# Kernel optimization log

Measured on AMD Instinct MI355X. Metric: run time of the kernel, lower is better.

Reference implementation:

```python
import jax, jax.numpy as jnp
import numpy as np

N_NODES = 100000
N_EDGES = 200000
D_LAT = 64
D_ENC = 32
N_FEAT = 2  # output features 'p', 'q'
D_IN = 2 * D_LAT + D_LAT + D_ENC + D_ENC  # 256
D_HID = 64


def setup_inputs() -> dict:
    key = jax.random.key(0)
    ks = jax.random.split(key, 12)
    return {
        "edge_array": jax.random.normal(ks[0], (N_EDGES, 4), dtype=jnp.float32),
        "h_local": jax.random.normal(ks[1], (N_NODES, D_LAT), dtype=jnp.float32),
        "h_global": jax.random.normal(ks[2], (1, D_LAT), dtype=jnp.float32),
        "enc_local": jax.random.normal(ks[3], (N_EDGES, D_ENC), dtype=jnp.float32),
        "enc_global": jax.random.normal(ks[4], (1, D_ENC), dtype=jnp.float32),
        "W1": jax.random.normal(ks[5], (N_FEAT, D_IN, D_HID), dtype=jnp.float32) / np.sqrt(D_IN),
        "b1": jnp.zeros((N_FEAT, D_HID), dtype=jnp.float32),
        "W2": jax.random.normal(ks[6], (N_FEAT, D_HID, D_HID), dtype=jnp.float32) / np.sqrt(D_HID),
        "b2": jnp.zeros((N_FEAT, D_HID), dtype=jnp.float32),
        "W3": jax.random.normal(ks[7], (N_FEAT, D_HID, 1), dtype=jnp.float32) / np.sqrt(D_HID),
        "b3": jnp.zeros((N_FEAT, 1), dtype=jnp.float32),
        "addr_from": jax.random.randint(ks[8], (N_EDGES,), 0, N_NODES, dtype=jnp.int32),
        "addr_to": jax.random.randint(ks[9], (N_EDGES,), 0, N_NODES, dtype=jnp.int32),
    }


def reference(edge_array, h_local, h_global, enc_local, enc_global,
              W1, b1, W2, b2, W3, b3, addr_from, addr_to):
    n = enc_local.shape[0]
    # gather node latents per address (drop/fill-0 semantics for out-of-range)
    g_from = h_local.at[addr_from].get(mode='fill', fill_value=0.0)  # [n, D_LAT]
    g_to = h_local.at[addr_to].get(mode='fill', fill_value=0.0)      # [n, D_LAT]
    # concat: [latents..., h_global*ones, enc_local, enc_global*ones]
    x = jnp.concatenate([
        g_from, g_to,
        jnp.broadcast_to(h_global, (n, h_global.shape[1])),
        enc_local,
        jnp.broadcast_to(enc_global, (n, enc_global.shape[1])),
    ], axis=1)  # [n, D_IN]
    # stacked per-feature MLPs (one MLP per output feature)
    h1 = jax.nn.leaky_relu(jnp.einsum('ni,fio->fno', x, W1) + b1[:, None, :])
    h2 = jax.nn.leaky_relu(jnp.einsum('fni,fio->fno', h1, W2) + b2[:, None, :])
    out = (jnp.einsum('fni,fio->fno', h2, W3) + b3[:, None, :])[..., 0]  # [F, n]
    isnan_mask = jnp.isnan(edge_array[:, 0])
    return jnp.where(isnan_mask[None, :], jnp.nan, out)
```

## Files before the change

kernel.cpp:

```cpp
#include <hip/hip_runtime.h>


#define OFF_W1 0
#define OFF_W2 40960
#define OFF_B1 57344
#define OFF_B2 57856
#define OFF_W3 58368
#define OFF_B3 58880
#define OFF_EA0 59392
#define NWAVE 8
#define LDS_TOTAL 58944
#define PREP_W_BLOCKS 114

typedef __attribute__((ext_vector_type(8))) short bf16x8;
typedef __attribute__((ext_vector_type(4))) float f32x4;

__device__ inline short f2bf(float f) {
    unsigned u = __builtin_bit_cast(unsigned, f);
    u += 0x7FFFu + ((u >> 16) & 1u);
    return (short)(u >> 16);
}

__device__ inline float4 ld4(const float* p, bool v) {
    if (v) return *(const float4*)p;
    return make_float4(0.f, 0.f, 0.f, 0.f);
}

__device__ inline unsigned cvt_pk(float lo, float hi) {
    unsigned r;
    asm("v_cvt_pk_bf16_f32 %0, %1, %2" : "=v"(r) : "v"(lo), "v"(hi));
    return r;
}

__device__ inline bf16x8 pack8(float4 a, float4 b) {
    union { bf16x8 v; unsigned u[4]; } r;
    r.u[0] = cvt_pk(a.x, a.y);
    r.u[1] = cvt_pk(a.z, a.w);
    r.u[2] = cvt_pk(b.x, b.y);
    r.u[3] = cvt_pk(b.z, b.w);
    return r.v;
}

__global__ void prep_all(const float* __restrict__ W1, const float* __restrict__ b1,
                         const float* __restrict__ W2, const float* __restrict__ b2,
                         const float* __restrict__ W3, const float* __restrict__ b3,
                         const float* __restrict__ h_global, const float* __restrict__ enc_global,
                         const float* __restrict__ edge_array, const float* __restrict__ h_local,
                         int n_edges, int n8,
                         float* __restrict__ ea0, short* __restrict__ hbf,
                         char* __restrict__ ws) {
    int b = blockIdx.x;
    if (b >= PREP_W_BLOCKS) {
        int rb = b - PREP_W_BLOCKS;
        int eb = (n_edges + 255) >> 8;
        if (rb < eb) {
            int e = rb * 256 + threadIdx.x;
            if (e < n_edges) ea0[e] = ((const float4*)edge_array)[e].x;
        } else {
            int i = (rb - eb) * 256 + threadIdx.x;
            if (i < n8) {
                float4 a = ((const float4*)h_local)[2 * i];
                float4 c = ((const float4*)h_local)[2 * i + 1];
                ((bf16x8*)hbf)[i] = pack8(a, c);
            } else if (i < n8 + 8) {
                ((bf16x8*)hbf)[i] = (bf16x8){0, 0, 0, 0, 0, 0, 0, 0};
            }
        }
        return;
    }
    int idx = b * 256 + threadIdx.x;
    short* w1f = (short*)(ws + OFF_W1);
    short* w2f = (short*)(ws + OFF_W2);
    float* bp1 = (float*)(ws + OFF_B1);
    float* bp2 = (float*)(ws + OFF_B2);
    float* wp3 = (float*)(ws + OFF_W3);
    float* bp3 = (float*)(ws + OFF_B3);
    if (idx < 20480) {
        int f = idx / 10240, r0 = idx % 10240;
        int kk = r0 / 2048, r1 = r0 % 2048;
        int mm = r1 / 512,  r2 = r1 % 512;
        int l = r2 / 8,     j = r2 % 8;
        int kt = kk * 32 + (l >> 4) * 8 + j;
        int r = (kt < 128) ? kt : kt + 64;
        int c = mm * 16 + (l & 15);
        w1f[idx] = f2bf(W1[(f * 256 + r) * 64 + c]);
    } else if (idx < 28672) {
        int i2 = idx - 20480;
        int f = i2 / 4096, r0 = i2 % 4096;
        int kk = r0 / 2048, r1 = r0 % 2048;
        int mm = r1 / 512,  r2 = r1 % 512;
        int l = r2 / 8,     j = r2 % 8;
        int k = kk * 32 + (l >> 4) * 8 + j;
        int c = mm * 16 + (l & 15);
        w2f[i2] = f2bf(W2[(f * 64 + k) * 64 + c]);
    } else if (idx < 28800) {
        int i3 = idx - 28672; int f = i3 / 64, o = i3 % 64;
        float s = b1[f * 64 + o];
        for (int t = 0; t < 64; ++t) s += h_global[t] * W1[(f * 256 + 128 + t) * 64 + o];
        for (int t = 0; t < 32; ++t) s += enc_global[t] * W1[(f * 256 + 224 + t) * 64 + o];
        bp1[i3] = s;
    } else if (idx < 28928) {
        int i4 = idx - 28800; bp2[i4] = b2[i4];
    } else if (idx < 29056) {
        int i5 = idx - 28928; wp3[i5] = W3[i5];
    } else if (idx < 29058) {
        bp3[idx - 29056] = b3[idx - 29056];
    }
}

struct Tile { bf16x8 a0, a1, a2, a3; float4 e0, e1; float ea; };

template<bool HBF>
__device__ inline void gather_tile(int tbase, int n_edges, int n_nodes,
        const int* __restrict__ addr_from, const int* __restrict__ addr_to,
        const float* __restrict__ h_local, const short* __restrict__ hbf,
        const float* __restrict__ enc_local, const float* __restrict__ edge_array,
        const float* __restrict__ ea0, int col16, int g, Tile& T) {
    int e = tbase + col16;
    if (HBF) {
        int ec = e < n_edges ? e : n_edges - 1;
        int af = addr_from[ec], at = addr_to[ec];
        unsigned ra = (unsigned)af < (unsigned)n_nodes ? (unsigned)af : (unsigned)n_nodes;
        unsigned rt = (unsigned)at < (unsigned)n_nodes ? (unsigned)at : (unsigned)n_nodes;
        const short* pf = hbf + (size_t)ra * 64 + g * 8;
        const short* pt = hbf + (size_t)rt * 64 + g * 8;
        T.a0 = *(const bf16x8*)pf; T.a1 = *(const bf16x8*)(pf + 32);
        T.a2 = *(const bf16x8*)pt; T.a3 = *(const bf16x8*)(pt + 32);
        const float* pe = enc_local + (size_t)ec * 32 + g * 8;
        T.e0 = *(const float4*)pe; T.e1 = *(const float4*)(pe + 4);
        T.ea = ea0[ec];
    } else {
        bool ev = e < n_edges;
        int af = ev ? addr_from[e] : -1;
        int at = ev ? addr_to[e] : -1;
        bool afv = (unsigned)af < (unsigned)n_nodes;
        bool atv = (unsigned)at < (unsigned)n_nodes;
        const float* pf = h_local + (size_t)(afv ? af : 0) * 64 + g * 8;
        const float* pt = h_local + (size_t)(atv ? at : 0) * 64 + g * 8;
        T.a0 = pack8(ld4(pf, afv),      ld4(pf + 4, afv));
        T.a1 = pack8(ld4(pf + 32, afv), ld4(pf + 36, afv));
        T.a2 = pack8(ld4(pt, atv),      ld4(pt + 4, atv));
        T.a3 = pack8(ld4(pt + 32, atv), ld4(pt + 36, atv));
        const float* pe = enc_local + (size_t)(ev ? e : 0) * 32 + g * 8;
        T.e0 = ld4(pe, ev); T.e1 = ld4(pe + 4, ev);
        T.ea = ev ? edge_array[4 * e] : 0.f;
    }
}

template<bool HBF>
__global__ __launch_bounds__(512, 4) void main_kernel(
        const float* __restrict__ edge_array, const float* __restrict__ h_local,
        const float* __restrict__ enc_local,
        const int* __restrict__ addr_from, const int* __restrict__ addr_to,
        const char* __restrict__ ws, const float* __restrict__ ea0,
        const short* __restrict__ hbf, float* __restrict__ out,
        int n_edges, int n_nodes) {
    __shared__ __align__(16) char lds[LDS_TOTAL];
    const int tid = threadIdx.x;
    const int lane = tid & 63, wave = tid >> 6;
    const int col16 = lane & 15, g = lane >> 4;
    const int g4 = g * 4;
    const bool hi = g >= 2;
    const int srcA = col16 + 32 * (g & 1);
    const int srcB = srcA + 16;
    const int ntiles = (n_edges + 15) >> 4;
    const int wstride = gridDim.x * NWAVE;

    int t = blockIdx.x * NWAVE + wave;
    bool valid = t < ntiles;
    Tile cur;
    if (valid)
        gather_tile<HBF>(t * 16, n_edges, n_nodes, addr_from, addr_to, h_local,
                         hbf, enc_local, edge_array, ea0, col16, g, cur);

    #pragma unroll
    for (int it = 0; it < 7; ++it)
        ((float4*)lds)[it * 512 + tid] = ((const float4*)ws)[it * 512 + tid];
    if (tid < 100)
        ((float4*)(lds + 57344))[tid] = ((const float4*)(ws + 57344))[tid];
    __syncthreads();

    const float b3v0 = ((const float*)(lds + OFF_B3))[0];
    const float b3v1 = ((const float*)(lds + OFF_B3))[1];

    while (valid) {
        bf16x8 a1[5] = {cur.a0, cur.a1, cur.a2, cur.a3, pack8(cur.e0, cur.e1)};
        float ea = cur.ea;
        int tb = t * 16;

        int tn = t + wstride;
        bool vnext = tn < ntiles;
        if (vnext)
            gather_tile<HBF>(tn * 16, n_edges, n_nodes, addr_from, addr_to, h_local,
                             hbf, enc_local, edge_array, ea0, col16, g, cur);

        #pragma unroll
        for (int f = 0; f < 2; ++f) {
            f32x4 acc1[4];
            #pragma unroll
            for (int mm = 0; mm < 4; ++mm)
                acc1[mm] = *(const f32x4*)(lds + OFF_B1 + (f * 64 + mm * 16 + g4) * 4);
            #pragma unroll
            for (int kk = 0; kk < 5; ++kk)
                #pragma unroll
                for (int mm = 0; mm < 4; ++mm) {
                    bf16x8 w = *(const bf16x8*)(lds + OFF_W1 + ((f * 5 + kk) * 4 + mm) * 1024 + lane * 16);
                    acc1[mm] = __builtin_amdgcn_mfma_f32_16x16x32_bf16(w, a1[kk], acc1[mm], 0, 0, 0);
                }

            unsigned pk[4][2];
            #pragma unroll
            for (int mm = 0; mm < 4; ++mm) {
                float v0 = acc1[mm][0], v1 = acc1[mm][1];
                float v2 = acc1[mm][2], v3 = acc1[mm][3];
                v0 = fmaxf(v0, 0.01f * v0); v1 = fmaxf(v1, 0.01f * v1);
                v2 = fmaxf(v2, 0.01f * v2); v3 = fmaxf(v3, 0.01f * v3);
                pk[mm][0] = cvt_pk(v0, v1);
                pk[mm][1] = cvt_pk(v2, v3);
            }

            f32x4 acc2[4];
            #pragma unroll
            for (int mm = 0; mm < 4; ++mm)
                acc2[mm] = *(const f32x4*)(lds + OFF_B2 + (f * 64 + mm * 16 + g4) * 4);
            #pragma unroll
            for (int kk2 = 0; kk2 < 2; ++kk2) {
                unsigned mL0 = pk[2 * kk2][0],     mL1 = pk[2 * kk2][1];
                unsigned mH0 = pk[2 * kk2 + 1][0], mH1 = pk[2 * kk2 + 1][1];
                unsigned t0L = (unsigned)__shfl((int)mL0, srcA, 64);
                unsigned t0H = (unsigned)__shfl((int)mH0, srcA, 64);
                unsigned t1L = (unsigned)__shfl((int)mL1, srcA, 64);
                unsigned t1H = (unsigned)__shfl((int)mH1, srcA, 64);
                unsigned t2L = (unsigned)__shfl((int)mL0, srcB, 64);
                unsigned t2H = (unsigned)__shfl((int)mH0, srcB, 64);
                unsigned t3L = (unsigned)__shfl((int)mL1, srcB, 64);
                unsigned t3H = (unsigned)__shfl((int)mH1, srcB, 64);
                union { bf16x8 v; unsigned u[4]; } bb;
                bb.u[0] = hi ? t0H : t0L;
                bb.u[1] = hi ? t1H : t1L;
                bb.u[2] = hi ? t2H : t2L;
                bb.u[3] = hi ? t3H : t3L;
                #pragma unroll
                for (int mm = 0; mm < 4; ++mm) {
                    bf16x8 w = *(const bf16x8*)(lds + OFF_W2 + ((f * 2 + kk2) * 4 + mm) * 1024 + lane * 16);
                    acc2[mm] = __builtin_amdgcn_mfma_f32_16x16x32_bf16(w, bb.v, acc2[mm], 0, 0, 0);
                }
            }

            float p = 0.f;
            #pragma unroll
            for (int mm = 0; mm < 4; ++mm) {
                f32x4 wv = *(const f32x4*)(lds + OFF_W3 + (f * 64 + mm * 16 + g4) * 4);
                #pragma unroll
                for (int jj = 0; jj < 4; ++jj) {
                    float h = acc2[mm][jj];
                    h = fmaxf(h, 0.01f * h);
                    p = fmaf(h, wv[jj], p);
                }
            }
            p += __shfl_xor(p, 16, 64);
            p += __shfl_xor(p, 32, 64);
            if (lane < 16) {
                int ee = tb + lane;
                if (ee < n_edges) {
                    float val = p + (f == 0 ? b3v0 : b3v1);
                    if (__builtin_isnan(ea)) val = __builtin_nanf("");
                    out[f * n_edges + ee] = val;
                }
            }
        }

        t = tn; valid = vnext;
    }
}

extern "C" void kernel_launch(void* const* d_in, const int* in_sizes, int n_in,
                              void* d_out, int out_size, void* d_ws, size_t ws_size,
                              hipStream_t stream) {
    const float* edge_array = (const float*)d_in[0];
    const float* h_local    = (const float*)d_in[1];
    const float* h_global   = (const float*)d_in[2];
    const float* enc_local  = (const float*)d_in[3];
    const float* enc_global = (const float*)d_in[4];
    const float* W1 = (const float*)d_in[5];
    const float* b1 = (const float*)d_in[6];
    const float* W2 = (const float*)d_in[7];
    const float* b2 = (const float*)d_in[8];
    const float* W3 = (const float*)d_in[9];
    const float* b3 = (const float*)d_in[10];
    const int* addr_from = (const int*)d_in[11];
    const int* addr_to   = (const int*)d_in[12];
    int n_edges = in_sizes[11];
    int n_nodes = in_sizes[1] / 64;
    int n8 = n_nodes * 8;
    char* ws = (char*)d_ws;

    size_t off_ea0 = OFF_EA0;
    size_t off_hbf = (off_ea0 + (size_t)n_edges * 4 + 255) & ~(size_t)255;
    size_t need = off_hbf + (size_t)(n_nodes + 1) * 128;
    bool use_hbf = ws_size >= need;
    float* ea0 = (float*)(ws + off_ea0);
    short* hbf = (short*)(ws + off_hbf);

    int eb = (n_edges + 255) / 256;
    int hb = (n8 + 8 + 255) / 256;
    int prep_blocks = PREP_W_BLOCKS + (use_hbf ? eb + hb : 0);
    hipLaunchKernelGGL(prep_all, dim3(prep_blocks), dim3(256), 0, stream,
                       W1, b1, W2, b2, W3, b3, h_global, enc_global,
                       edge_array, h_local, n_edges, n8, ea0, hbf, ws);

    int ntiles = (n_edges + 15) / 16;
    int nblk = 512;
    if (nblk * NWAVE > ntiles) nblk = (ntiles + NWAVE - 1) / NWAVE;
    if (use_hbf) {
        hipLaunchKernelGGL((main_kernel<true>), dim3(nblk), dim3(512), 0, stream,
                           edge_array, h_local, enc_local, addr_from, addr_to,
                           ws, ea0, hbf, (float*)d_out, n_edges, n_nodes);
    } else {
        hipLaunchKernelGGL((main_kernel<false>), dim3(nblk), dim3(512), 0, stream,
                           edge_array, h_local, enc_local, addr_from, addr_to,
                           ws, ea0, hbf, (float*)d_out, n_edges, n_nodes);
    }
}
```

Measured before the change: 37.24 us.

## Switch MLP to 32x32x16 MFMA tiles with 32-edge wave tiles

Moves the per-wave MLP from 16x16x32 to 32x32x16 bf16 MFMA, so each wave processes 32 edges per iteration. The W1 and W2 pre-swizzle layouts change to match, and the layer-2 operand exchange is reduced to xor-32 shuffles. The prefetch now covers only the address indices for the next tile, and the node rows are loaded in the current iteration, which may expose more gather latency. Accumulator register use grows, and ea0 is now always prepared, even on the fallback path.

```diff
diff --git a/kernel.cpp b/kernel.cpp
--- a/kernel.cpp
+++ b/kernel.cpp
@@ -14,6 +14,7 @@
 
 typedef __attribute__((ext_vector_type(8))) short bf16x8;
 typedef __attribute__((ext_vector_type(4))) float f32x4;
+typedef __attribute__((ext_vector_type(16))) float f32x16;
 
 __device__ inline short f2bf(float f) {
     unsigned u = __builtin_bit_cast(unsigned, f);
@@ -40,6 +41,8 @@
     r.u[3] = cvt_pk(b.z, b.w);
     return r.v;
 }
+
+__device__ inline float lrelu(float x) { return fmaxf(x, 0.01f * x); }
 
 __global__ void prep_all(const float* __restrict__ W1, const float* __restrict__ b1,
                          const float* __restrict__ W2, const float* __restrict__ b2,
@@ -77,21 +80,21 @@
     float* bp3 = (float*)(ws + OFF_B3);
     if (idx < 20480) {
         int f = idx / 10240, r0 = idx % 10240;
-        int kk = r0 / 2048, r1 = r0 % 2048;
+        int kk = r0 / 1024, r1 = r0 % 1024;
         int mm = r1 / 512,  r2 = r1 % 512;
         int l = r2 / 8,     j = r2 % 8;
-        int kt = kk * 32 + (l >> 4) * 8 + j;
+        int kt = kk * 16 + (l >> 5) * 8 + j;
         int r = (kt < 128) ? kt : kt + 64;
-        int c = mm * 16 + (l & 15);
+        int c = mm * 32 + (l & 31);
         w1f[idx] = f2bf(W1[(f * 256 + r) * 64 + c]);
     } else if (idx < 28672) {
         int i2 = idx - 20480;
         int f = i2 / 4096, r0 = i2 % 4096;
-        int kk = r0 / 2048, r1 = r0 % 2048;
+        int kk2 = r0 / 1024, r1 = r0 % 1024;
         int mm = r1 / 512,  r2 = r1 % 512;
         int l = r2 / 8,     j = r2 % 8;
-        int k = kk * 32 + (l >> 4) * 8 + j;
-        int c = mm * 16 + (l & 15);
+        int k = kk2 * 16 + (l >> 5) * 8 + j;
+        int c = mm * 32 + (l & 31);
         w2f[i2] = f2bf(W2[(f * 64 + k) * 64 + c]);
     } else if (idx < 28800) {
         int i3 = idx - 28672; int f = i3 / 64, o = i3 % 64;
@@ -108,49 +111,9 @@
     }
 }
 
-struct Tile { bf16x8 a0, a1, a2, a3; float4 e0, e1; float ea; };
-
-template<bool HBF>
-__device__ inline void gather_tile(int tbase, int n_edges, int n_nodes,
-        const int* __restrict__ addr_from, const int* __restrict__ addr_to,
-        const float* __restrict__ h_local, const short* __restrict__ hbf,
-        const float* __restrict__ enc_local, const float* __restrict__ edge_array,
-        const float* __restrict__ ea0, int col16, int g, Tile& T) {
-    int e = tbase + col16;
-    if (HBF) {
-        int ec = e < n_edges ? e : n_edges - 1;
-        int af = addr_from[ec], at = addr_to[ec];
-        unsigned ra = (unsigned)af < (unsigned)n_nodes ? (unsigned)af : (unsigned)n_nodes;
-        unsigned rt = (unsigned)at < (unsigned)n_nodes ? (unsigned)at : (unsigned)n_nodes;
-        const short* pf = hbf + (size_t)ra * 64 + g * 8;
-        const short* pt = hbf + (size_t)rt * 64 + g * 8;
-        T.a0 = *(const bf16x8*)pf; T.a1 = *(const bf16x8*)(pf + 32);
-        T.a2 = *(const bf16x8*)pt; T.a3 = *(const bf16x8*)(pt + 32);
-        const float* pe = enc_local + (size_t)ec * 32 + g * 8;
-        T.e0 = *(const float4*)pe; T.e1 = *(const float4*)(pe + 4);
-        T.ea = ea0[ec];
-    } else {
-        bool ev = e < n_edges;
-        int af = ev ? addr_from[e] : -1;
-        int at = ev ? addr_to[e] : -1;
-        bool afv = (unsigned)af < (unsigned)n_nodes;
-        bool atv = (unsigned)at < (unsigned)n_nodes;
-        const float* pf = h_local + (size_t)(afv ? af : 0) * 64 + g * 8;
-        const float* pt = h_local + (size_t)(atv ? at : 0) * 64 + g * 8;
-        T.a0 = pack8(ld4(pf, afv),      ld4(pf + 4, afv));
-        T.a1 = pack8(ld4(pf + 32, afv), ld4(pf + 36, afv));
-        T.a2 = pack8(ld4(pt, atv),      ld4(pt + 4, atv));
-        T.a3 = pack8(ld4(pt + 32, atv), ld4(pt + 36, atv));
-        const float* pe = enc_local + (size_t)(ev ? e : 0) * 32 + g * 8;
-        T.e0 = ld4(pe, ev); T.e1 = ld4(pe + 4, ev);
-        T.ea = ev ? edge_array[4 * e] : 0.f;
-    }
-}
-
 template<bool HBF>
 __global__ __launch_bounds__(512, 4) void main_kernel(
-        const float* __restrict__ edge_array, const float* __restrict__ h_local,
-        const float* __restrict__ enc_local,
+        const float* __restrict__ h_local, const float* __restrict__ enc_local,
         const int* __restrict__ addr_from, const int* __restrict__ addr_to,
         const char* __restrict__ ws, const float* __restrict__ ea0,
         const short* __restrict__ hbf, float* __restrict__ out,
@@ -158,20 +121,17 @@
     __shared__ __align__(16) char lds[LDS_TOTAL];
     const int tid = threadIdx.x;
     const int lane = tid & 63, wave = tid >> 6;
-    const int col16 = lane & 15, g = lane >> 4;
-    const int g4 = g * 4;
-    const bool hi = g >= 2;
-    const int srcA = col16 + 32 * (g & 1);
-    const int srcB = srcA + 16;
-    const int ntiles = (n_edges + 15) >> 4;
-    const int wstride = gridDim.x * NWAVE;
+    const int col = lane & 31, hi = lane >> 5;
+    const int niters = (n_edges + 31) >> 5;
+    const int stride = gridDim.x * NWAVE;
 
     int t = blockIdx.x * NWAVE + wave;
-    bool valid = t < ntiles;
-    Tile cur;
-    if (valid)
-        gather_tile<HBF>(t * 16, n_edges, n_nodes, addr_from, addr_to, h_local,
-                         hbf, enc_local, edge_array, ea0, col16, g, cur);
+    bool valid = t < niters;
+    int af = 0, at = 0;
+    if (valid) {
+        int ec0 = t * 32 + col; if (ec0 >= n_edges) ec0 = n_edges - 1;
+        af = addr_from[ec0]; at = addr_to[ec0];
+    }
 
     #pragma unroll
     for (int it = 0; it < 7; ++it)
@@ -184,84 +144,120 @@
     const float b3v1 = ((const float*)(lds + OFF_B3))[1];
 
     while (valid) {
-        bf16x8 a1[5] = {cur.a0, cur.a1, cur.a2, cur.a3, pack8(cur.e0, cur.e1)};
-        float ea = cur.ea;
-        int tb = t * 16;
-
-        int tn = t + wstride;
-        bool vnext = tn < ntiles;
-        if (vnext)
-            gather_tile<HBF>(tn * 16, n_edges, n_nodes, addr_from, addr_to, h_local,
-                             hbf, enc_local, edge_array, ea0, col16, g, cur);
+        int tb = t * 32;
+        int ec = tb + col; if (ec >= n_edges) ec = n_edges - 1;
+
+        bf16x8 a1[10];
+        float4 e0, e1, e2, e3;
+        float ea;
+        if (HBF) {
+            unsigned ra = (unsigned)af < (unsigned)n_nodes ? (unsigned)af : (unsigned)n_nodes;
+            unsigned rt = (unsigned)at < (unsigned)n_nodes ? (unsigned)at : (unsigned)n_nodes;
+            const short* pf = hbf + (size_t)ra * 64 + hi * 8;
+            const short* pt = hbf + (size_t)rt * 64 + hi * 8;
+            a1[0] = *(const bf16x8*)pf;        a1[1] = *(const bf16x8*)(pf + 16);
+            a1[2] = *(const bf16x8*)(pf + 32); a1[3] = *(const bf16x8*)(pf + 48);
+            a1[4] = *(const bf16x8*)pt;        a1[5] = *(const bf16x8*)(pt + 16);
+            a1[6] = *(const bf16x8*)(pt + 32); a1[7] = *(const bf16x8*)(pt + 48);
+            const float* pe = enc_local + (size_t)ec * 32 + hi * 8;
+            e0 = *(const float4*)pe;        e1 = *(const float4*)(pe + 4);
+            e2 = *(const float4*)(pe + 16); e3 = *(const float4*)(pe + 20);
+            ea = ea0[ec];
+        } else {
+            bool afv = (unsigned)af < (unsigned)n_nodes;
+            bool atv = (unsigned)at < (unsigned)n_nodes;
+            const float* pf = h_local + (size_t)(afv ? af : 0) * 64 + hi * 8;
+            const float* pt = h_local + (size_t)(atv ? at : 0) * 64 + hi * 8;
+            #pragma unroll
+            for (int kk = 0; kk < 4; ++kk) {
+                a1[kk]     = pack8(ld4(pf + 16 * kk, afv), ld4(pf + 16 * kk + 4, afv));
+                a1[kk + 4] = pack8(ld4(pt + 16 * kk, atv), ld4(pt + 16 * kk + 4, atv));
+            }
+            const float* pe = enc_local + (size_t)ec * 32 + hi * 8;
+            e0 = *(const float4*)pe;        e1 = *(const float4*)(pe + 4);
+            e2 = *(const float4*)(pe + 16); e3 = *(const float4*)(pe + 20);
+            ea = ea0[ec];
+        }
+
+        int tn = t + stride;
+        bool vnext = tn < niters;
+        int af2 = 0, at2 = 0;
+        if (vnext) {
+            int ec2 = tn * 32 + col; if (ec2 >= n_edges) ec2 = n_edges - 1;
+            af2 = addr_from[ec2]; at2 = addr_to[ec2];
+        }
+
+        a1[8] = pack8(e0, e1);
+        a1[9] = pack8(e2, e3);
 
         #pragma unroll
         for (int f = 0; f < 2; ++f) {
-            f32x4 acc1[4];
-            #pragma unroll
-            for (int mm = 0; mm < 4; ++mm)
-                acc1[mm] = *(const f32x4*)(lds + OFF_B1 + (f * 64 + mm * 16 + g4) * 4);
-            #pragma unroll
-            for (int kk = 0; kk < 5; ++kk)
-                #pragma unroll
-                for (int mm = 0; mm < 4; ++mm) {
-                    bf16x8 w = *(const bf16x8*)(lds + OFF_W1 + ((f * 5 + kk) * 4 + mm) * 1024 + lane * 16);
-                    acc1[mm] = __builtin_amdgcn_mfma_f32_16x16x32_bf16(w, a1[kk], acc1[mm], 0, 0, 0);
-                }
-
-            unsigned pk[4][2];
-            #pragma unroll
-            for (int mm = 0; mm < 4; ++mm) {
-                float v0 = acc1[mm][0], v1 = acc1[mm][1];
-                float v2 = acc1[mm][2], v3 = acc1[mm][3];
-                v0 = fmaxf(v0, 0.01f * v0); v1 = fmaxf(v1, 0.01f * v1);
-                v2 = fmaxf(v2, 0.01f * v2); v3 = fmaxf(v3, 0.01f * v3);
-                pk[mm][0] = cvt_pk(v0, v1);
-                pk[mm][1] = cvt_pk(v2, v3);
+            f32x16 acc[2];
+            #pragma unroll
+            for (int mm = 0; mm < 2; ++mm)
+                #pragma unroll
+                for (int q2 = 0; q2 < 4; ++q2) {
+                    f32x4 v = *(const f32x4*)(lds + OFF_B1 + (f * 64 + mm * 32 + q2 * 8 + hi * 4) * 4);
+                    acc[mm][q2 * 4 + 0] = v[0]; acc[mm][q2 * 4 + 1] = v[1];
+                    acc[mm][q2 * 4 + 2] = v[2]; acc[mm][q2 * 4 + 3] = v[3];
+                }
+            #pragma unroll
+            for (int kk = 0; kk < 10; ++kk)
+                #pragma unroll
+                for (int mm = 0; mm < 2; ++mm) {
+                    bf16x8 w = *(const bf16x8*)(lds + OFF_W1 + (((f * 10 + kk) * 2 + mm) * 64 + lane) * 16);
+                    acc[mm] = __builtin_amdgcn_mfma_f32_32x32x16_bf16(w, a1[kk], acc[mm], 0, 0, 0);
+                }
+
+            unsigned pk[2][8];
+            #pragma unroll
+            for (int mm = 0; mm < 2; ++mm)
+                #pragma unroll
+                for (int i = 0; i < 8; ++i)
+                    pk[mm][i] = cvt_pk(lrelu(acc[mm][2 * i]), lrelu(acc[mm][2 * i + 1]));
+
+            f32x16 acc2[2];
+            #pragma unroll
+            for (int mm = 0; mm < 2; ++mm)
+                #pragma unroll
+                for (int q2 = 0; q2 < 4; ++q2) {
+                    f32x4 v = *(const f32x4*)(lds + OFF_B2 + (f * 64 + mm * 32 + q2 * 8 + hi * 4) * 4);
+                    acc2[mm][q2 * 4 + 0] = v[0]; acc2[mm][q2 * 4 + 1] = v[1];
+                    acc2[mm][q2 * 4 + 2] = v[2]; acc2[mm][q2 * 4 + 3] = v[3];
+                }
+            #pragma unroll
+            for (int kk2 = 0; kk2 < 4; ++kk2) {
+                const int ms = kk2 >> 1, c = (kk2 & 1) * 4;
+                unsigned pass0 = hi ? pk[ms][c + 0] : pk[ms][c + 2];
+                unsigned pass1 = hi ? pk[ms][c + 1] : pk[ms][c + 3];
+                unsigned sw0 = (unsigned)__shfl_xor((int)pass0, 32, 64);
+                unsigned sw1 = (unsigned)__shfl_xor((int)pass1, 32, 64);
+                union { bf16x8 v; unsigned u[4]; } bb;
+                bb.u[0] = hi ? sw0 : pk[ms][c + 0];
+                bb.u[1] = hi ? sw1 : pk[ms][c + 1];
+                bb.u[2] = hi ? pk[ms][c + 2] : sw0;
+                bb.u[3] = hi ? pk[ms][c + 3] : sw1;
+                #pragma unroll
+                for (int mm = 0; mm < 2; ++mm) {
+                    bf16x8 w = *(const bf16x8*)(lds + OFF_W2 + (((f * 4 + kk2) * 2 + mm) * 64 + lane) * 16);
+                    acc2[mm] = __builtin_amdgcn_mfma_f32_32x32x16_bf16(w, bb.v, acc2[mm], 0, 0, 0);
+                }
             }
 
-            f32x4 acc2[4];
-            #pragma unroll
-            for (int mm = 0; mm < 4; ++mm)
-                acc2[mm] = *(const f32x4*)(lds + OFF_B2 + (f * 64 + mm * 16 + g4) * 4);
-            #pragma unroll
-            for (int kk2 = 0; kk2 < 2; ++kk2) {
-                unsigned mL0 = pk[2 * kk2][0],     mL1 = pk[2 * kk2][1];
-                unsigned mH0 = pk[2 * kk2 + 1][0], mH1 = pk[2 * kk2 + 1][1];
-                unsigned t0L = (unsigned)__shfl((int)mL0, srcA, 64);
-                unsigned t0H = (unsigned)__shfl((int)mH0, srcA, 64);
-                unsigned t1L = (unsigned)__shfl((int)mL1, srcA, 64);
-                unsigned t1H = (unsigned)__shfl((int)mH1, srcA, 64);
-                unsigned t2L = (unsigned)__shfl((int)mL0, srcB, 64);
-                unsigned t2H = (unsigned)__shfl((int)mH0, srcB, 64);
-                unsigned t3L = (unsigned)__shfl((int)mL1, srcB, 64);
-                unsigned t3H = (unsigned)__shfl((int)mH1, srcB, 64);
-                union { bf16x8 v; unsigned u[4]; } bb;
-                bb.u[0] = hi ? t0H : t0L;
-                bb.u[1] = hi ? t1H : t1L;
-                bb.u[2] = hi ? t2H : t2L;
-                bb.u[3] = hi ? t3H : t3L;
-                #pragma unroll
-                for (int mm = 0; mm < 4; ++mm) {
-                    bf16x8 w = *(const bf16x8*)(lds + OFF_W2 + ((f * 2 + kk2) * 4 + mm) * 1024 + lane * 16);
-                    acc2[mm] = __builtin_amdgcn_mfma_f32_16x16x32_bf16(w, bb.v, acc2[mm], 0, 0, 0);
-                }
-            }
-
             float p = 0.f;
             #pragma unroll
-            for (int mm = 0; mm < 4; ++mm) {
-                f32x4 wv = *(const f32x4*)(lds + OFF_W3 + (f * 64 + mm * 16 + g4) * 4);
-                #pragma unroll
-                for (int jj = 0; jj < 4; ++jj) {
-                    float h = acc2[mm][jj];
-                    h = fmaxf(h, 0.01f * h);
-                    p = fmaf(h, wv[jj], p);
-                }
-            }
-            p += __shfl_xor(p, 16, 64);
+            for (int mm = 0; mm < 2; ++mm)
+                #pragma unroll
+                for (int q2 = 0; q2 < 4; ++q2) {
+                    f32x4 wv = *(const f32x4*)(lds + OFF_W3 + (f * 64 + mm * 32 + q2 * 8 + hi * 4) * 4);
+                    #pragma unroll
+                    for (int j = 0; j < 4; ++j)
+                        p = fmaf(lrelu(acc2[mm][q2 * 4 + j]), wv[j], p);
+                }
             p += __shfl_xor(p, 32, 64);
-            if (lane < 16) {
-                int ee = tb + lane;
+
+            if (lane < 32) {
+                int ee = tb + col;
                 if (ee < n_edges) {
                     float val = p + (f == 0 ? b3v0 : b3v1);
                     if (__builtin_isnan(ea)) val = __builtin_nanf("");
@@ -270,7 +266,7 @@
             }
         }
 
-        t = tn; valid = vnext;
+        t = tn; valid = vnext; af = af2; at = at2;
     }
 }
 
@@ -304,21 +300,21 @@
 
     int eb = (n_edges + 255) / 256;
     int hb = (n8 + 8 + 255) / 256;
-    int prep_blocks = PREP_W_BLOCKS + (use_hbf ? eb + hb : 0);
+    int prep_blocks = PREP_W_BLOCKS + eb + (use_hbf ? hb : 0);
     hipLaunchKernelGGL(prep_all, dim3(prep_blocks), dim3(256), 0, stream,
                        W1, b1, W2, b2, W3, b3, h_global, enc_global,
-                       edge_array, h_local, n_edges, n8, ea0, hbf, ws);
-
-    int ntiles = (n_edges + 15) / 16;
+                       edge_array, h_local, n_edges, use_hbf ? n8 : 0, ea0, hbf, ws);
+
+    int niters = (n_edges + 31) / 32;
     int nblk = 512;
-    if (nblk * NWAVE > ntiles) nblk = (ntiles + NWAVE - 1) / NWAVE;
+    if (nblk * NWAVE > niters) nblk = (niters + NWAVE - 1) / NWAVE;
     if (use_hbf) {
         hipLaunchKernelGGL((main_kernel<true>), dim3(nblk), dim3(512), 0, stream,
-                           edge_array, h_local, enc_local, addr_from, addr_to,
+                           h_local, enc_local, addr_from, addr_to,
                            ws, ea0, hbf, (float*)d_out, n_edges, n_nodes);
     } else {
         hipLaunchKernelGGL((main_kernel<false>), dim3(nblk), dim3(512), 0, stream,
-                           edge_array, h_local, enc_local, addr_from, addr_to,
+                           h_local, enc_local, addr_from, addr_to,
                            ws, ea0, hbf, (float*)d_out, n_edges, n_nodes);
     }
 }
```

Result: faster. 35.75 us (-4.0%).
